# Kernel tuning notes

Measured on AMD Instinct MI355X. Metric: run time of the kernel, lower is better.

The kernel has to match this reference:

```python
import jax, jax.numpy as jnp
import numpy as np

B, S, H, NH = 8, 2048, 128, 4
HS = H // NH
EPS = 1e-8


def setup_inputs() -> dict:
    key = jax.random.key(0)
    ks = jax.random.split(key, 20)
    sc = 1.0 / np.sqrt(H)
    d = {
        'item_embeds': jax.random.normal(ks[0], (B, S, H), jnp.float32),
        'behavior_embeds': jax.random.normal(ks[1], (B, S, H), jnp.float32),
        'attn_mask': jnp.zeros((B, 1, S, S), jnp.float32),
    }
    names = ['Wq', 'Wk', 'Wv', 'Wqb', 'Wkb', 'Wvb', 'Wf']
    for i, n in enumerate(names):
        d[n] = jax.random.normal(ks[2 + i], (H, H), jnp.float32) * sc
        d['b' + n[1:]] = jnp.zeros((H,), jnp.float32)
    d['ln_w'] = jnp.ones((H,), jnp.float32)
    d['ln_b'] = jnp.zeros((H,), jnp.float32)
    return d


def _split_heads(x):
    # [B,S,H] -> [B,NH,S,HS]
    return x.reshape(B, S, NH, HS).transpose(0, 2, 1, 3)


def _layer_norm(x, w, b):
    u = jnp.mean(x, -1, keepdims=True)
    s = jnp.mean((x - u) ** 2, -1, keepdims=True)
    return w * ((x - u) / jnp.sqrt(s + EPS)) + b


def reference(item_embeds, behavior_embeds, attn_mask,
              Wq, bq, Wk, bk, Wv, bv,
              Wqb, bqb, Wkb, bkb, Wvb, bvb,
              Wf, bf, ln_w, ln_b):
    Q = _split_heads(item_embeds @ Wq + bq)
    K = _split_heads(item_embeds @ Wk + bk)
    V = _split_heads(item_embeds @ Wv + bv)
    Qb = _split_heads(behavior_embeds @ Wqb + bqb)
    Kb = _split_heads(behavior_embeds @ Wkb + bkb)
    # V_behavior computed in the original forward but unused downstream
    _Vb = _split_heads(behavior_embeds @ Wvb + bvb)
    scores = (jnp.einsum('bhqd,bhkd->bhqk', Q, K)
              + jnp.einsum('bhqd,bhkd->bhqk', Qb, Kb)) / np.sqrt(HS)
    scores = scores + attn_mask
    probs = jax.nn.softmax(scores, axis=-1)
    attn_out = jnp.einsum('bhqk,bhkd->bhqd', probs, V)
    attn_out = attn_out.transpose(0, 2, 1, 3).reshape(B, S, H)
    out = attn_out @ Wf + bf
    return _layer_norm(out + item_embeds, ln_w, ln_b)
```

## Files before the change

### kernel.cpp

```cpp
#include <hip/hip_runtime.h>
#include <math.h>

typedef unsigned short ushort_t;
typedef __attribute__((ext_vector_type(8))) short bf16x8;
typedef __attribute__((ext_vector_type(4))) float f32x4;

namespace {
constexpr int B = 8, S = 2048, H = 128, NH = 4, HS = 32;
constexpr float EPS = 1e-8f;
constexpr float SCALE = 0.17677669529663687f;
constexpr int QT = 16, KT = 64;
constexpr int NE = B * S * H;
constexpr int NML = B * NH * S;
}

__device__ __forceinline__ ushort_t f2bf(float f) {
  unsigned u = __float_as_uint(f);
  unsigned r = (u + 0x7FFFu + ((u >> 16) & 1u)) >> 16;
  return (ushort_t)r;
}

__device__ __forceinline__ float bf2f(ushort_t u) {
  return __uint_as_float((unsigned)u << 16);
}

__device__ __forceinline__ f32x4 mfma16(bf16x8 a, bf16x8 b, f32x4 c) {
  return __builtin_amdgcn_mfma_f32_16x16x32_bf16(a, b, c, 0, 0, 0);
}

__global__ __launch_bounds__(256) void wcvt_kernel(
    const float* __restrict__ Wq, const float* __restrict__ Wk, const float* __restrict__ Wv,
    const float* __restrict__ Wqb, const float* __restrict__ Wkb, const float* __restrict__ Wf,
    ushort_t* __restrict__ Wt)
{
  const float* Ws[6] = {Wq, Wk, Wv, Wqb, Wkb, Wf};
  const float scl[6] = {SCALE, 1.f, 1.f, SCALE, 1.f, 1.f};
  const int m = blockIdx.y;
  const int kb = blockIdx.x;
  const float* W = Ws[m];
  const float sc = scl[m];
  __shared__ float T[32 * 132];
  const int t = threadIdx.x;
#pragma unroll
  for (int u = 0; u < 4; ++u) {
    const int idx = u * 256 + t;
    const int row = idx >> 5, c4 = idx & 31;
    const float4 v = *(const float4*)&W[(kb * 32 + row) * H + c4 * 4];
    *(float4*)&T[row * 132 + c4 * 4] = v;
  }
  __syncthreads();
#pragma unroll
  for (int u = 0; u < 16; ++u) {
    const int idx = u * 256 + t;
    const int n = idx >> 5, kk = idx & 31;
    Wt[m * (H * H) + n * H + kb * 32 + kk] = f2bf(T[kk * 132 + n] * sc);
  }
}

__global__ __launch_bounds__(256) void proj_kernel(
    const float* __restrict__ item, const float* __restrict__ beh,
    const ushort_t* __restrict__ Wt,
    const float* __restrict__ bq, const float* __restrict__ bk, const float* __restrict__ bv,
    const float* __restrict__ bqb, const float* __restrict__ bkb,
    ushort_t* __restrict__ Qo, ushort_t* __restrict__ Ko, ushort_t* __restrict__ Qbo,
    ushort_t* __restrict__ Kbo, ushort_t* __restrict__ Vto)
{
  __shared__ ushort_t Xs[32 * 136];
  __shared__ ushort_t Yb[32 * 136];
  const int t = threadIdx.x;
  const int p = blockIdx.y;
  const long r0 = (long)blockIdx.x * 32;
  const float* X = (p < 3) ? item : beh;
#pragma unroll
  for (int u = 0; u < 4; ++u) {
    const int idx = u * 256 + t;
    const int row = idx >> 5, c4 = idx & 31;
    const float4 v = *(const float4*)&X[(r0 + row) * H + c4 * 4];
    unsigned long long pk = (unsigned long long)f2bf(v.x) | ((unsigned long long)f2bf(v.y) << 16)
        | ((unsigned long long)f2bf(v.z) << 32) | ((unsigned long long)f2bf(v.w) << 48);
    *(unsigned long long*)&Xs[row * 136 + c4 * 4] = pk;
  }
  __syncthreads();

  const int w = t >> 6, l = t & 63, l15 = l & 15, quad = l >> 4;
  const int bb = (int)(r0 >> 11);
  const int s0 = (int)(r0 & (S - 1));
  const float* bias[5] = {bq, bk, bv, bqb, bkb};
  const float bscale[5] = {SCALE, 1.f, 1.f, SCALE, 1.f};
  ushort_t* dsts[5] = {Qo, Ko, Vto, Qbo, Kbo};

  bf16x8 af[2][4];
#pragma unroll
  for (int mt = 0; mt < 2; ++mt)
#pragma unroll
    for (int ks = 0; ks < 4; ++ks)
      af[mt][ks] = *(const bf16x8*)&Xs[(mt * 16 + l15) * 136 + ks * 32 + quad * 8];

  f32x4 acc[2][2];
#pragma unroll
  for (int nt = 0; nt < 2; ++nt) {
    const float bcol = bias[p][w * 32 + nt * 16 + l15] * bscale[p];
#pragma unroll
    for (int mt = 0; mt < 2; ++mt)
      acc[mt][nt] = (f32x4){bcol, bcol, bcol, bcol};
  }
  const ushort_t* Wp = Wt + p * (H * H);
#pragma unroll
  for (int ks = 0; ks < 4; ++ks) {
    bf16x8 bfr[2];
#pragma unroll
    for (int nt = 0; nt < 2; ++nt)
      bfr[nt] = *(const bf16x8*)&Wp[(w * 32 + nt * 16 + l15) * H + ks * 32 + quad * 8];
#pragma unroll
    for (int mt = 0; mt < 2; ++mt)
#pragma unroll
      for (int nt = 0; nt < 2; ++nt)
        acc[mt][nt] = mfma16(af[mt][ks], bfr[nt], acc[mt][nt]);
  }
#pragma unroll
  for (int mt = 0; mt < 2; ++mt)
#pragma unroll
    for (int nt = 0; nt < 2; ++nt)
#pragma unroll
      for (int r = 0; r < 4; ++r)
        Yb[(mt * 16 + quad * 4 + r) * 136 + w * 32 + nt * 16 + l15] = f2bf(acc[mt][nt][r]);
  __syncthreads();
  ushort_t* dst = dsts[p];
  if (p == 2) {
    const int d = t >> 1, sh = (t & 1) * 16;
    ushort_t tmp[16];
#pragma unroll
    for (int i = 0; i < 16; ++i) tmp[i] = Yb[(sh + i) * 136 + d];
    const long gidx = ((long)(bb * NH + (d >> 5)) * HS + (d & 31)) * S + s0 + sh;
    *(uint4*)&dst[gidx] = *(const uint4*)&tmp[0];
    *(uint4*)&dst[gidx + 8] = *(const uint4*)&tmp[8];
  } else {
    const int row = t >> 3, cb = (t & 7) * 16;
    const int h = cb >> 5, dd = cb & 31;
    const long gidx = ((long)(bb * NH + h) * S + s0 + row) * HS + dd;
    *(uint4*)&dst[gidx] = *(const uint4*)&Yb[row * 136 + cb];
    *(uint4*)&dst[gidx + 8] = *(const uint4*)&Yb[row * 136 + cb + 8];
  }
}

__global__ __launch_bounds__(256, 3) void attn_kernel(
    const ushort_t* __restrict__ Q, const ushort_t* __restrict__ K,
    const ushort_t* __restrict__ Qb, const ushort_t* __restrict__ Kb,
    const ushort_t* __restrict__ Vt, const float* __restrict__ mask,
    ushort_t* __restrict__ Op, float* __restrict__ Mp, float* __restrict__ Lp)
{
  __shared__ ushort_t Pb[NH][2][16 * 72];
  const int t = threadIdx.x;
  const int w = t >> 6;
  const int l = t & 63, l15 = l & 15, quad = l >> 4, quad4 = quad * 4;
  const int q0 = blockIdx.x * 32;
  const int b = blockIdx.y;
  const int half_ = blockIdx.z;
  const long hQ = (long)(b * NH + w) * S * HS;
  const long hV = (long)(b * NH + w) * HS * S;
  const ushort_t* Kp  = K + hQ;
  const ushort_t* Kbp = Kb + hQ;
  const ushort_t* Vp  = Vt + hV;

  bf16x8 qf[2], qbf[2];
#pragma unroll
  for (int c = 0; c < 2; ++c) {
    qf[c]  = *(const bf16x8*)&Q[hQ + (long)(q0 + c * 16 + l15) * HS + quad * 8];
    qbf[c] = *(const bf16x8*)&Qb[hQ + (long)(q0 + c * 16 + l15) * HS + quad * 8];
  }

  const float* mrow[2][4];
#pragma unroll
  for (int c = 0; c < 2; ++c)
#pragma unroll
    for (int r = 0; r < 4; ++r)
      mrow[c][r] = mask + ((long)b * S + q0 + c * 16 + quad4 + r) * S + l15;

  float mold[2][4], lsum[2][4];
  f32x4 O[2][2];
#pragma unroll
  for (int c = 0; c < 2; ++c) {
#pragma unroll
    for (int r = 0; r < 4; ++r) { mold[c][r] = -1e30f; lsum[c][r] = 0.f; }
#pragma unroll
    for (int dt = 0; dt < 2; ++dt) O[c][dt] = (f32x4){0.f, 0.f, 0.f, 0.f};
  }

  const int kt0 = half_ * (S / KT / 2), kt1 = kt0 + (S / KT / 2);
  for (int kt = kt0; kt < kt1; ++kt) {
    const int k0 = kt * KT;
    bf16x8 kf[4], kbf[4];
#pragma unroll
    for (int nt = 0; nt < 4; ++nt) {
      kf[nt]  = *(const bf16x8*)&Kp[(long)(k0 + nt * 16 + l15) * HS + quad * 8];
      kbf[nt] = *(const bf16x8*)&Kbp[(long)(k0 + nt * 16 + l15) * HS + quad * 8];
    }
    f32x4 sc[2][4];
#pragma unroll
    for (int c = 0; c < 2; ++c)
#pragma unroll
      for (int nt = 0; nt < 4; ++nt)
#pragma unroll
        for (int r = 0; r < 4; ++r)
          sc[c][nt][r] = mrow[c][r][k0 + nt * 16];
#pragma unroll
    for (int c = 0; c < 2; ++c)
#pragma unroll
      for (int nt = 0; nt < 4; ++nt) {
        sc[c][nt] = mfma16(qbf[c], kbf[nt], sc[c][nt]);
        sc[c][nt] = mfma16(qf[c], kf[nt], sc[c][nt]);
      }
    bf16x8 vf[2][2];
#pragma unroll
    for (int dt = 0; dt < 2; ++dt)
#pragma unroll
      for (int ks = 0; ks < 2; ++ks)
        vf[dt][ks] = *(const bf16x8*)&Vp[(long)(dt * 16 + l15) * S + k0 + ks * 32 + quad * 8];
#pragma unroll
    for (int c = 0; c < 2; ++c) {
      float alpha[4];
#pragma unroll
      for (int r = 0; r < 4; ++r) {
        float rm = fmaxf(fmaxf(sc[c][0][r], sc[c][1][r]), fmaxf(sc[c][2][r], sc[c][3][r]));
        rm = fmaxf(rm, __shfl_xor(rm, 1));
        rm = fmaxf(rm, __shfl_xor(rm, 2));
        rm = fmaxf(rm, __shfl_xor(rm, 4));
        rm = fmaxf(rm, __shfl_xor(rm, 8));
        const float mnew = fmaxf(mold[c][r], rm);
        alpha[r] = __expf(mold[c][r] - mnew);
        float rs = 0.f;
#pragma unroll
        for (int nt = 0; nt < 4; ++nt) {
          const float p = __expf(sc[c][nt][r] - mnew);
          sc[c][nt][r] = p;
          rs += p;
        }
        rs += __shfl_xor(rs, 1);
        rs += __shfl_xor(rs, 2);
        rs += __shfl_xor(rs, 4);
        rs += __shfl_xor(rs, 8);
        lsum[c][r] = lsum[c][r] * alpha[r] + rs;
        mold[c][r] = mnew;
      }
#pragma unroll
      for (int dt = 0; dt < 2; ++dt)
#pragma unroll
        for (int r = 0; r < 4; ++r)
          O[c][dt][r] *= alpha[r];
      ushort_t* Pw = Pb[w][c];
#pragma unroll
      for (int nt = 0; nt < 4; ++nt)
#pragma unroll
        for (int r = 0; r < 4; ++r)
          Pw[(quad4 + r) * 72 + nt * 16 + l15] = f2bf(sc[c][nt][r]);
    }
#pragma unroll
    for (int c = 0; c < 2; ++c) {
      const ushort_t* Pw = Pb[w][c];
      bf16x8 pf[2];
#pragma unroll
      for (int ks = 0; ks < 2; ++ks)
        pf[ks] = *(const bf16x8*)&Pw[l15 * 72 + ks * 32 + quad * 8];
#pragma unroll
      for (int dt = 0; dt < 2; ++dt)
#pragma unroll
        for (int ks = 0; ks < 2; ++ks)
          O[c][dt] = mfma16(pf[ks], vf[dt][ks], O[c][dt]);
    }
  }
#pragma unroll
  for (int c = 0; c < 2; ++c) {
#pragma unroll
    for (int r = 0; r < 4; ++r) {
      const float inv = 1.f / lsum[c][r];
      const long row = (long)b * S + q0 + c * 16 + quad4 + r;
#pragma unroll
      for (int dt = 0; dt < 2; ++dt)
        Op[(long)half_ * NE + row * H + w * 32 + dt * 16 + l15] = f2bf(O[c][dt][r] * inv);
    }
    if (l15 == 0) {
#pragma unroll
      for (int r = 0; r < 4; ++r) {
        const long idx = ((long)(half_ * B + b) * NH + w) * S + q0 + c * 16 + quad4 + r;
        Mp[idx] = mold[c][r];
        Lp[idx] = lsum[c][r];
      }
    }
  }
}

__global__ __launch_bounds__(256) void out_kernel(
    const ushort_t* __restrict__ Op, const float* __restrict__ Mp, const float* __restrict__ Lp,
    const float* __restrict__ item,
    const ushort_t* __restrict__ Wft, const float* __restrict__ bf_,
    const float* __restrict__ lnw, const float* __restrict__ lnb,
    float* __restrict__ out)
{
  __shared__ ushort_t As[16 * 136];
  __shared__ float Ys[16 * 132];
  const int t = threadIdx.x;
  const long r0 = (long)blockIdx.x * 16;
  {
    const int row = t >> 4, c8 = t & 15;
    const long g = r0 + row;
    const int bb = (int)(g >> 11);
    const int ss = (int)(g & (S - 1));
    const int col0 = c8 * 8;
    const int h = col0 >> 5;
    const long mlidx = ((long)bb * NH + h) * S + ss;
    const float m1 = Mp[mlidx], m2 = Mp[(long)NML + mlidx];
    const float l1 = Lp[mlidx], l2 = Lp[(long)NML + mlidx];
    const float M = fmaxf(m1, m2);
    const float w1 = l1 * __expf(m1 - M), w2 = l2 * __expf(m2 - M);
    const float inv = 1.f / (w1 + w2);
    const float wa = w1 * inv, wb = w2 * inv;
    const uint4 a1 = *(const uint4*)&Op[g * H + col0];
    const uint4 a2 = *(const uint4*)&Op[(long)NE + g * H + col0];
    const ushort_t* p1 = (const ushort_t*)&a1;
    const ushort_t* p2 = (const ushort_t*)&a2;
    ushort_t mg[8];
#pragma unroll
    for (int i = 0; i < 8; ++i)
      mg[i] = f2bf(bf2f(p1[i]) * wa + bf2f(p2[i]) * wb);
    *(uint4*)&As[row * 136 + col0] = *(const uint4*)&mg[0];
  }
  __syncthreads();
  const int w = t >> 6, l = t & 63, l15 = l & 15, quad = l >> 4;
  f32x4 acc[2];
#pragma unroll
  for (int nt = 0; nt < 2; ++nt) {
    const float bcol = bf_[w * 32 + nt * 16 + l15];
    acc[nt] = (f32x4){bcol, bcol, bcol, bcol};
  }
#pragma unroll
  for (int ks = 0; ks < 4; ++ks) {
    const bf16x8 a = *(const bf16x8*)&As[l15 * 136 + ks * 32 + quad * 8];
#pragma unroll
    for (int nt = 0; nt < 2; ++nt) {
      const bf16x8 bfr = *(const bf16x8*)&Wft[(w * 32 + nt * 16 + l15) * H + ks * 32 + quad * 8];
      acc[nt] = mfma16(a, bfr, acc[nt]);
    }
  }
#pragma unroll
  for (int nt = 0; nt < 2; ++nt)
#pragma unroll
    for (int r = 0; r < 4; ++r) {
      const int rl = quad * 4 + r;
      const int col = w * 32 + nt * 16 + l15;
      Ys[rl * 132 + col] = acc[nt][r] + item[(r0 + rl) * H + col];
    }
  __syncthreads();
  const int rl = t >> 4, ch = t & 15;
  float v[8];
#pragma unroll
  for (int g = 0; g < 2; ++g) {
    const float4 y = *(const float4*)&Ys[rl * 132 + ch * 8 + g * 4];
    v[g * 4 + 0] = y.x; v[g * 4 + 1] = y.y; v[g * 4 + 2] = y.z; v[g * 4 + 3] = y.w;
  }
  float s = 0.f;
#pragma unroll
  for (int i = 0; i < 8; ++i) s += v[i];
  s += __shfl_xor(s, 1);
  s += __shfl_xor(s, 2);
  s += __shfl_xor(s, 4);
  s += __shfl_xor(s, 8);
  const float u_ = s * (1.f / H);
  float s2 = 0.f;
#pragma unroll
  for (int i = 0; i < 8; ++i) { const float d = v[i] - u_; s2 += d * d; }
  s2 += __shfl_xor(s2, 1);
  s2 += __shfl_xor(s2, 2);
  s2 += __shfl_xor(s2, 4);
  s2 += __shfl_xor(s2, 8);
  const float rinv = rsqrtf(s2 * (1.f / H) + EPS);
#pragma unroll
  for (int g = 0; g < 2; ++g) {
    float4 o;
    const int col = ch * 8 + g * 4;
    o.x = lnw[col + 0] * ((v[g * 4 + 0] - u_) * rinv) + lnb[col + 0];
    o.y = lnw[col + 1] * ((v[g * 4 + 1] - u_) * rinv) + lnb[col + 1];
    o.z = lnw[col + 2] * ((v[g * 4 + 2] - u_) * rinv) + lnb[col + 2];
    o.w = lnw[col + 3] * ((v[g * 4 + 3] - u_) * rinv) + lnb[col + 3];
    *(float4*)&out[(r0 + rl) * H + col] = o;
  }
}

extern "C" void kernel_launch(void* const* d_in, const int* in_sizes, int n_in,
                              void* d_out, int out_size, void* d_ws, size_t ws_size,
                              hipStream_t stream) {
  const float* item = (const float*)d_in[0];
  const float* beh  = (const float*)d_in[1];
  const float* mask = (const float*)d_in[2];
  const float* Wq  = (const float*)d_in[3];  const float* bq  = (const float*)d_in[4];
  const float* Wk  = (const float*)d_in[5];  const float* bk  = (const float*)d_in[6];
  const float* Wv  = (const float*)d_in[7];  const float* bv  = (const float*)d_in[8];
  const float* Wqb = (const float*)d_in[9];  const float* bqb = (const float*)d_in[10];
  const float* Wkb = (const float*)d_in[11]; const float* bkb = (const float*)d_in[12];
  const float* Wf  = (const float*)d_in[15]; const float* bfv = (const float*)d_in[16];
  const float* lnw = (const float*)d_in[17]; const float* lnb = (const float*)d_in[18];
  float* out = (float*)d_out;

  ushort_t* ws = (ushort_t*)d_ws;
  ushort_t* Qw   = ws;
  ushort_t* Kw   = Qw + NE;
  ushort_t* Qbw  = Kw + NE;
  ushort_t* Kbw  = Qbw + NE;
  ushort_t* Vtw  = Kbw + NE;
  ushort_t* Opw  = Vtw + NE;
  ushort_t* Wt   = Opw + 2 * (long)NE;
  float* Mpw = (float*)(Wt + 6 * H * H);
  float* Lpw = Mpw + 2 * (long)NML;

  wcvt_kernel<<<dim3(4, 6), 256, 0, stream>>>(Wq, Wk, Wv, Wqb, Wkb, Wf, Wt);
  proj_kernel<<<dim3((B * S) / 32, 5), 256, 0, stream>>>(
      item, beh, Wt, bq, bk, bv, bqb, bkb, Qw, Kw, Qbw, Kbw, Vtw);
  attn_kernel<<<dim3(S / 32, B, 2), 256, 0, stream>>>(
      Qw, Kw, Qbw, Kbw, Vtw, mask, Opw, Mpw, Lpw);
  out_kernel<<<dim3((B * S) / 16), 256, 0, stream>>>(
      Opw, Mpw, Lpw, item, Wt + 5 * H * H, bfv, lnw, lnb, out);
}
```

Measured before the change: 362.4 us.

## Stage attention mask tiles through double-buffered LDS with coalesced float4 loads

The attention mask used to be read straight from global memory as scalar loads scattered across 8 row pointers per lane. It is now loaded cooperatively as coalesced float4 chunks into a double-buffered shared tile, with the next tile prefetched into registers during the current iteration. V fragment loads are moved earlier to overlap with the score compute, and the occupancy hint rises from 3 to 4 blocks. The cost is a block-wide barrier every iteration, more LDS use that could limit occupancy, and extra register pressure from the staged values.

```diff
diff --git a/kernel.cpp b/kernel.cpp
--- a/kernel.cpp
+++ b/kernel.cpp
@@ -12,6 +12,7 @@
 constexpr int QT = 16, KT = 64;
 constexpr int NE = B * S * H;
 constexpr int NML = B * NH * S;
+constexpr int MSTRIDE = 68;
 }
 
 __device__ __forceinline__ ushort_t f2bf(float f) {
@@ -143,13 +144,14 @@
   }
 }
 
-__global__ __launch_bounds__(256, 3) void attn_kernel(
+__global__ __launch_bounds__(256, 4) void attn_kernel(
     const ushort_t* __restrict__ Q, const ushort_t* __restrict__ K,
     const ushort_t* __restrict__ Qb, const ushort_t* __restrict__ Kb,
     const ushort_t* __restrict__ Vt, const float* __restrict__ mask,
     ushort_t* __restrict__ Op, float* __restrict__ Mp, float* __restrict__ Lp)
 {
   __shared__ ushort_t Pb[NH][2][16 * 72];
+  __shared__ float Msk[2][32 * MSTRIDE];
   const int t = threadIdx.x;
   const int w = t >> 6;
   const int l = t & 63, l15 = l & 15, quad = l >> 4, quad4 = quad * 4;
@@ -169,12 +171,13 @@
     qbf[c] = *(const bf16x8*)&Qb[hQ + (long)(q0 + c * 16 + l15) * HS + quad * 8];
   }
 
-  const float* mrow[2][4];
-#pragma unroll
-  for (int c = 0; c < 2; ++c)
-#pragma unroll
-    for (int r = 0; r < 4; ++r)
-      mrow[c][r] = mask + ((long)b * S + q0 + c * 16 + quad4 + r) * S + l15;
+  const float* mb[2];
+  int mlw[2];
+#pragma unroll
+  for (int u = 0; u < 2; ++u) {
+    mb[u] = mask + ((long)b * S + q0 + u * 16 + (t >> 4)) * S + (t & 15) * 4;
+    mlw[u] = (u * 16 + (t >> 4)) * MSTRIDE + (t & 15) * 4;
+  }
 
   float mold[2][4], lsum[2][4];
   f32x4 O[2][2];
@@ -187,7 +190,16 @@
   }
 
   const int kt0 = half_ * (S / KT / 2), kt1 = kt0 + (S / KT / 2);
+  {
+    const int k00 = kt0 * KT;
+#pragma unroll
+    for (int u = 0; u < 2; ++u)
+      *(float4*)&Msk[0][mlw[u]] = *(const float4*)&mb[u][k00];
+  }
+  __syncthreads();
+
   for (int kt = kt0; kt < kt1; ++kt) {
+    const int buf = (kt - kt0) & 1;
     const int k0 = kt * KT;
     bf16x8 kf[4], kbf[4];
 #pragma unroll
@@ -195,14 +207,28 @@
       kf[nt]  = *(const bf16x8*)&Kp[(long)(k0 + nt * 16 + l15) * HS + quad * 8];
       kbf[nt] = *(const bf16x8*)&Kbp[(long)(k0 + nt * 16 + l15) * HS + quad * 8];
     }
+    bf16x8 vf[2][2];
+#pragma unroll
+    for (int dt = 0; dt < 2; ++dt)
+#pragma unroll
+      for (int ks = 0; ks < 2; ++ks)
+        vf[dt][ks] = *(const bf16x8*)&Vp[(long)(dt * 16 + l15) * S + k0 + ks * 32 + quad * 8];
+    const bool havestage = (kt + 1 < kt1);
+    float4 stg[2];
+    if (havestage) {
+#pragma unroll
+      for (int u = 0; u < 2; ++u)
+        stg[u] = *(const float4*)&mb[u][k0 + KT];
+    }
     f32x4 sc[2][4];
+    const float* Mb = &Msk[buf][0];
 #pragma unroll
     for (int c = 0; c < 2; ++c)
 #pragma unroll
       for (int nt = 0; nt < 4; ++nt)
 #pragma unroll
         for (int r = 0; r < 4; ++r)
-          sc[c][nt][r] = mrow[c][r][k0 + nt * 16];
+          sc[c][nt][r] = Mb[(c * 16 + quad4 + r) * MSTRIDE + nt * 16 + l15];
 #pragma unroll
     for (int c = 0; c < 2; ++c)
 #pragma unroll
@@ -210,12 +236,6 @@
         sc[c][nt] = mfma16(qbf[c], kbf[nt], sc[c][nt]);
         sc[c][nt] = mfma16(qf[c], kf[nt], sc[c][nt]);
       }
-    bf16x8 vf[2][2];
-#pragma unroll
-    for (int dt = 0; dt < 2; ++dt)
-#pragma unroll
-      for (int ks = 0; ks < 2; ++ks)
-        vf[dt][ks] = *(const bf16x8*)&Vp[(long)(dt * 16 + l15) * S + k0 + ks * 32 + quad * 8];
 #pragma unroll
     for (int c = 0; c < 2; ++c) {
       float alpha[4];
@@ -267,6 +287,12 @@
         for (int ks = 0; ks < 2; ++ks)
           O[c][dt] = mfma16(pf[ks], vf[dt][ks], O[c][dt]);
     }
+    if (havestage) {
+#pragma unroll
+      for (int u = 0; u < 2; ++u)
+        *(float4*)&Msk[buf ^ 1][mlw[u]] = stg[u];
+    }
+    __syncthreads();
   }
 #pragma unroll
   for (int c = 0; c < 2; ++c) {
```

After: 479.9 us. 1.32x slower.

## Stage attention mask tiles through double-buffered shared memory shared across head-waves

Applied to the files above, without the earlier changes.

Before this change, each of the four waves (one per head) loaded the same 32x64 mask tile from global memory with strided scalar reads. Now the whole block loads each mask tile once with float4 loads into a double-buffered LDS array, prefetching the next tile into registers during compute. Waves then read the mask from LDS. This cuts redundant global mask traffic by about 4x and coalesces the loads, at the cost of extra LDS use (about 17KB, which may lower occupancy below 3 blocks per CU) and a block-wide barrier every KV tile.

```diff
diff --git a/kernel.cpp b/kernel.cpp
--- a/kernel.cpp
+++ b/kernel.cpp
@@ -12,6 +12,7 @@
 constexpr int QT = 16, KT = 64;
 constexpr int NE = B * S * H;
 constexpr int NML = B * NH * S;
+constexpr int MSTRIDE = 68;
 }
 
 __device__ __forceinline__ ushort_t f2bf(float f) {
@@ -150,6 +151,7 @@
     ushort_t* __restrict__ Op, float* __restrict__ Mp, float* __restrict__ Lp)
 {
   __shared__ ushort_t Pb[NH][2][16 * 72];
+  __shared__ __align__(16) float Msk[2][32 * MSTRIDE];
   const int t = threadIdx.x;
   const int w = t >> 6;
   const int l = t & 63, l15 = l & 15, quad = l >> 4, quad4 = quad * 4;
@@ -169,12 +171,11 @@
     qbf[c] = *(const bf16x8*)&Qb[hQ + (long)(q0 + c * 16 + l15) * HS + quad * 8];
   }
 
-  const float* mrow[2][4];
-#pragma unroll
-  for (int c = 0; c < 2; ++c)
-#pragma unroll
-    for (int r = 0; r < 4; ++r)
-      mrow[c][r] = mask + ((long)b * S + q0 + c * 16 + quad4 + r) * S + l15;
+  const int srow = t >> 4, scol = (t & 15) * 4;
+  const float* mb0 = mask + ((long)b * S + q0 + srow) * S + scol;
+  const float* mb1 = mb0 + 16 * (long)S;
+  const int mlw0 = srow * MSTRIDE + scol;
+  const int mlw1 = (16 + srow) * MSTRIDE + scol;
 
   float mold[2][4], lsum[2][4];
   f32x4 O[2][2];
@@ -187,14 +188,22 @@
   }
 
   const int kt0 = half_ * (S / KT / 2), kt1 = kt0 + (S / KT / 2);
-  for (int kt = kt0; kt < kt1; ++kt) {
-    const int k0 = kt * KT;
+  *(float4*)&Msk[0][mlw0] = *(const float4*)&mb0[kt0 * KT];
+  *(float4*)&Msk[0][mlw1] = *(const float4*)&mb1[kt0 * KT];
+  __syncthreads();
+
+  auto step = [&](const float* cur, float* nxt, int k0, bool pre) {
     bf16x8 kf[4], kbf[4];
 #pragma unroll
     for (int nt = 0; nt < 4; ++nt) {
       kf[nt]  = *(const bf16x8*)&Kp[(long)(k0 + nt * 16 + l15) * HS + quad * 8];
       kbf[nt] = *(const bf16x8*)&Kbp[(long)(k0 + nt * 16 + l15) * HS + quad * 8];
     }
+    float4 stg0, stg1;
+    if (pre) {
+      stg0 = *(const float4*)&mb0[k0 + KT];
+      stg1 = *(const float4*)&mb1[k0 + KT];
+    }
     f32x4 sc[2][4];
 #pragma unroll
     for (int c = 0; c < 2; ++c)
@@ -202,7 +211,7 @@
       for (int nt = 0; nt < 4; ++nt)
 #pragma unroll
         for (int r = 0; r < 4; ++r)
-          sc[c][nt][r] = mrow[c][r][k0 + nt * 16];
+          sc[c][nt][r] = cur[(c * 16 + quad4 + r) * MSTRIDE + nt * 16 + l15];
 #pragma unroll
     for (int c = 0; c < 2; ++c)
 #pragma unroll
@@ -267,7 +276,18 @@
         for (int ks = 0; ks < 2; ++ks)
           O[c][dt] = mfma16(pf[ks], vf[dt][ks], O[c][dt]);
     }
-  }
+    if (pre) {
+      *(float4*)&nxt[mlw0] = stg0;
+      *(float4*)&nxt[mlw1] = stg1;
+    }
+    __syncthreads();
+  };
+
+  for (int kt = kt0; kt < kt1; kt += 2) {
+    step(&Msk[0][0], &Msk[1][0], kt * KT, true);
+    step(&Msk[1][0], &Msk[0][0], (kt + 1) * KT, kt + 2 < kt1);
+  }
+
 #pragma unroll
   for (int c = 0; c < 2; ++c) {
 #pragma unroll
```

Result: faster. 347.3 us (-4.2%).
